# Kernel tuning notes

Measured on AMD Instinct MI355X. Metric: run time of the kernel, lower is better.

The kernel has to match this reference:

```python
import jax, jax.numpy as jnp
import numpy as np

TAU_PLUS = 0.02
TAU_MINUS = 0.02
TAU_X = 0.101
A_TRIPLET = 0.0065
HOMEOSTATIC_RATE = 0.1
DT = 0.001
SPIKE_P = 0.05  # spike probability used to binarize inputs


def setup_inputs() -> dict:
    key = jax.random.key(0)
    k1, k2, k3 = jax.random.split(key, 3)
    B, P, Q, T = 16, 2048, 2048, 256
    pre_spikes = (jax.random.uniform(k1, (B, P, T)) < SPIKE_P).astype(jnp.float32)
    post_spikes = (jax.random.uniform(k2, (B, Q, T)) < SPIKE_P).astype(jnp.float32)
    weights = jax.random.normal(k3, (P, Q), dtype=jnp.float32) * 0.1
    meta_A_plus = jnp.float32(0.01)
    meta_A_minus = jnp.float32(0.012)
    return {"pre_spikes": pre_spikes, "post_spikes": post_spikes,
            "weights": weights, "meta_A_plus": meta_A_plus,
            "meta_A_minus": meta_A_minus}


def _traces(spikes_tbn, decay):
    """Trace value used at step t: x_t = decay * (x_{t-1} + s_{t-1}), x_0 = 0."""
    def step(carry, s):
        x = decay * carry          # decayed trace, used for this step's update
        return x + s, x            # spike added AFTER the update, per original
    init = jnp.zeros(spikes_tbn.shape[1:], spikes_tbn.dtype)
    _, xs = jax.lax.scan(step, init, spikes_tbn)
    return xs  # [T, B, N]


def reference(pre_spikes, post_spikes, weights, meta_A_plus, meta_A_minus):
    B, P, T = pre_spikes.shape
    exp_plus = jnp.exp(jnp.float32(-DT / TAU_PLUS))
    exp_minus = jnp.exp(jnp.float32(-DT / TAU_MINUS))
    exp_x = jnp.exp(jnp.float32(-DT / TAU_X))

    pre_t = jnp.transpose(pre_spikes, (2, 0, 1))    # [T, B, P]
    post_t = jnp.transpose(post_spikes, (2, 0, 1))  # [T, B, Q]

    x_pre = _traces(pre_t, exp_plus)     # [T, B, P]
    x_post = _traces(post_t, exp_minus)  # [T, B, Q]
    x_trip = _traces(post_t, exp_x)      # [T, B, Q]

    # Per-step outer products summed over time == one big contraction over (t, b).
    ltp = jnp.einsum('tbp,tbq->pq', x_pre, post_t) * meta_A_plus
    triplet = jnp.einsum('tbp,tbq->pq', x_pre, post_t * x_trip) * A_TRIPLET
    ltd = jnp.einsum('tbp,tbq->pq', pre_t, x_post) * meta_A_minus
    weight_updates = ltp + triplet - ltd

    # Homeostatic scaling (fresh module: activity history holds only this sample)
    current_activity = (pre_spikes.sum() + post_spikes.sum()) / (B * T)
    scaling_factor = jnp.sqrt(HOMEOSTATIC_RATE / (current_activity + 1e-6))

    updated_weights = weights + weight_updates * scaling_factor
    return jnp.clip(updated_weights, -2.0, 2.0)
```

## Files before the change

### kernel.cpp

```cpp
#include <hip/hip_runtime.h>


constexpr int TB = 16;
constexpr int NP = 2048;
constexpr int NQ = 2048;
constexpr int TT = 256;
constexpr int KH = TB * TT;
constexpr int KT = 2 * KH;

typedef unsigned short ushort_t;
typedef __attribute__((ext_vector_type(8))) __bf16 bf16x8;
typedef __attribute__((ext_vector_type(4))) float f32x4;

__device__ __forceinline__ unsigned bf1(float f) {
    unsigned u = __builtin_bit_cast(unsigned, f);
    return (u + 0x7FFFu + ((u >> 16) & 1u)) >> 16;
}
__device__ __forceinline__ unsigned pack2(float lo, float hi) {
    return bf1(lo) | (bf1(hi) << 16);
}
__device__ __forceinline__ unsigned spk2(float a, float b) {
    return ((a != 0.f) ? 0x3F80u : 0u) | ((b != 0.f) ? 0x3F800000u : 0u);
}

constexpr float DF1 = 0.95122942450071400910f;
constexpr float DF2 = DF1 * DF1;
constexpr float DF4 = DF2 * DF2;
constexpr float DF8 = DF4 * DF4;
constexpr float DF16 = DF8 * DF8;
constexpr float DF32 = DF16 * DF16;
constexpr float DF64 = DF32 * DF32;

constexpr float DX1 = 0.99014786386058731819f;
constexpr float DX2 = DX1 * DX1;
constexpr float DX4 = DX2 * DX2;
constexpr float DX8 = DX4 * DX4;
constexpr float DX16 = DX8 * DX8;
constexpr float DX32 = DX16 * DX16;
constexpr float DX64 = DX32 * DX32;

template <int K>
__device__ __forceinline__ float seg_step(float b, float pw, int sl) {
    float t = __shfl_up(b, K, 64);
    return (sl >= K) ? fmaf(pw, t, b) : b;
}
__device__ __forceinline__ float scan16(float c, float p1, float p2, float p4,
                                        float p8, int sl) {
    c = seg_step<1>(c, p1, sl);
    c = seg_step<2>(c, p2, sl);
    c = seg_step<4>(c, p4, sl);
    c = seg_step<8>(c, p8, sl);
    return c;
}
__device__ __forceinline__ float fold4(float4 u, float d) {
    float C = d * u.x;
    C = d * (C + u.y); C = d * (C + u.z); C = d * (C + u.w);
    return C;
}
__device__ __forceinline__ float4 expand4(float x, float4 u, float d) {
    float4 t;
    t.x = x; x = d * (x + u.x);
    t.y = x; x = d * (x + u.y);
    t.z = x; x = d * (x + u.z);
    t.w = x;
    return t;
}

__global__ __launch_bounds__(256) void stage_traces(
    const float* __restrict__ pre, const float* __restrict__ post,
    const float* __restrict__ mApP, const float* __restrict__ mAmP,
    ushort_t* __restrict__ Ab, ushort_t* __restrict__ Bb,
    float* __restrict__ partials)
{
    const int tid  = threadIdx.x;
    const int lane = tid & 63;
    const int wv   = tid >> 6;
    const int sl   = lane & 15;
    const int rowg = blockIdx.x * 16 + wv * 4 + (lane >> 4);
    const bool isPre = rowg < TB * NP;
    const int m = isPre ? rowg : rowg - TB * NP;
    const int b = m >> 11;
    const int r = m & 2047;

    const float4* srcRow = (const float4*)((isPre ? pre : post) + (size_t)m * TT);
    const float4 u0 = srcRow[sl];
    const float4 u1 = srcRow[16 + sl];
    const float4 u2 = srcRow[32 + sl];
    const float4 u3 = srcRow[48 + sl];

    float cnt = ((u0.x + u0.y) + (u0.z + u0.w)) + ((u1.x + u1.y) + (u1.z + u1.w))
              + ((u2.x + u2.y) + (u2.z + u2.w)) + ((u3.x + u3.y) + (u3.z + u3.w));

    const int hi = lane | 15;

    float bf0 = scan16(fold4(u0, DF1), DF4, DF8, DF16, DF32, sl);
    float bf1_ = scan16(fold4(u1, DF1), DF4, DF8, DF16, DF32, sl);
    float bf2 = scan16(fold4(u2, DF1), DF4, DF8, DF16, DF32, sl);
    float bf3 = scan16(fold4(u3, DF1), DF4, DF8, DF16, DF32, sl);
    const float Tf0 = __shfl(bf0, hi, 64);
    const float Tf1 = __shfl(bf1_, hi, 64);
    const float Tf2 = __shfl(bf2, hi, 64);
    const float Xf1 = Tf0;
    const float Xf2 = fmaf(DF64, Xf1, Tf1);
    const float Xf3 = fmaf(DF64, Xf2, Tf2);
    float ef0 = __shfl_up(bf0, 1, 64);
    float ef1 = __shfl_up(bf1_, 1, 64);
    float ef2 = __shfl_up(bf2, 1, 64);
    float ef3 = __shfl_up(bf3, 1, 64);
    if (sl == 0) { ef0 = 0.f; ef1 = 0.f; ef2 = 0.f; ef3 = 0.f; }
    float pf = 1.f;
    if (sl & 1) pf *= DF4;
    if (sl & 2) pf *= DF8;
    if (sl & 4) pf *= DF16;
    if (sl & 8) pf *= DF32;
    const float4 t0 = expand4(ef0,                 u0, DF1);
    const float4 t1 = expand4(fmaf(pf, Xf1, ef1),  u1, DF1);
    const float4 t2 = expand4(fmaf(pf, Xf2, ef2),  u2, DF1);
    const float4 t3 = expand4(fmaf(pf, Xf3, ef3),  u3, DF1);

    ushort_t* oA = (isPre ? Ab : Bb) + (size_t)r * KT + b * TT + 4 * sl;

    if (isPre) {
        *(uint2*)(oA)            = uint2{pack2(t0.x, t0.y), pack2(t0.z, t0.w)};
        *(uint2*)(oA + 64)       = uint2{pack2(t1.x, t1.y), pack2(t1.z, t1.w)};
        *(uint2*)(oA + 128)      = uint2{pack2(t2.x, t2.y), pack2(t2.z, t2.w)};
        *(uint2*)(oA + 192)      = uint2{pack2(t3.x, t3.y), pack2(t3.z, t3.w)};
        *(uint2*)(oA + KH)       = uint2{spk2(u0.x, u0.y), spk2(u0.z, u0.w)};
        *(uint2*)(oA + KH + 64)  = uint2{spk2(u1.x, u1.y), spk2(u1.z, u1.w)};
        *(uint2*)(oA + KH + 128) = uint2{spk2(u2.x, u2.y), spk2(u2.z, u2.w)};
        *(uint2*)(oA + KH + 192) = uint2{spk2(u3.x, u3.y), spk2(u3.z, u3.w)};
    } else {
        float bx0 = scan16(fold4(u0, DX1), DX4, DX8, DX16, DX32, sl);
        float bx1 = scan16(fold4(u1, DX1), DX4, DX8, DX16, DX32, sl);
        float bx2 = scan16(fold4(u2, DX1), DX4, DX8, DX16, DX32, sl);
        float bx3 = scan16(fold4(u3, DX1), DX4, DX8, DX16, DX32, sl);
        const float Tx0 = __shfl(bx0, hi, 64);
        const float Tx1 = __shfl(bx1, hi, 64);
        const float Tx2 = __shfl(bx2, hi, 64);
        const float Xx1 = Tx0;
        const float Xx2 = fmaf(DX64, Xx1, Tx1);
        const float Xx3 = fmaf(DX64, Xx2, Tx2);
        float ex0 = __shfl_up(bx0, 1, 64);
        float ex1 = __shfl_up(bx1, 1, 64);
        float ex2 = __shfl_up(bx2, 1, 64);
        float ex3 = __shfl_up(bx3, 1, 64);
        if (sl == 0) { ex0 = 0.f; ex1 = 0.f; ex2 = 0.f; ex3 = 0.f; }
        float px = 1.f;
        if (sl & 1) px *= DX4;
        if (sl & 2) px *= DX8;
        if (sl & 4) px *= DX16;
        if (sl & 8) px *= DX32;
        const float4 w0 = expand4(ex0,                u0, DX1);
        const float4 w1 = expand4(fmaf(px, Xx1, ex1), u1, DX1);
        const float4 w2 = expand4(fmaf(px, Xx2, ex2), u2, DX1);
        const float4 w3 = expand4(fmaf(px, Xx3, ex3), u3, DX1);

        const float Ap = *mApP;
        const float Am = *mAmP;
        auto av2 = [&](float sa, float ta, float sb, float tb) -> unsigned {
            unsigned lo = (sa != 0.f) ? bf1(fmaf(0.0065f, ta, Ap)) : 0u;
            unsigned hi2 = (sb != 0.f) ? bf1(fmaf(0.0065f, tb, Ap)) : 0u;
            return lo | (hi2 << 16);
        };
        *(uint2*)(oA)       = uint2{av2(u0.x, w0.x, u0.y, w0.y), av2(u0.z, w0.z, u0.w, w0.w)};
        *(uint2*)(oA + 64)  = uint2{av2(u1.x, w1.x, u1.y, w1.y), av2(u1.z, w1.z, u1.w, w1.w)};
        *(uint2*)(oA + 128) = uint2{av2(u2.x, w2.x, u2.y, w2.y), av2(u2.z, w2.z, u2.w, w2.w)};
        *(uint2*)(oA + 192) = uint2{av2(u3.x, w3.x, u3.y, w3.y), av2(u3.z, w3.z, u3.w, w3.w)};
        *(uint2*)(oA + KH)       = uint2{pack2(-Am * t0.x, -Am * t0.y), pack2(-Am * t0.z, -Am * t0.w)};
        *(uint2*)(oA + KH + 64)  = uint2{pack2(-Am * t1.x, -Am * t1.y), pack2(-Am * t1.z, -Am * t1.w)};
        *(uint2*)(oA + KH + 128) = uint2{pack2(-Am * t2.x, -Am * t2.y), pack2(-Am * t2.z, -Am * t2.w)};
        *(uint2*)(oA + KH + 192) = uint2{pack2(-Am * t3.x, -Am * t3.y), pack2(-Am * t3.z, -Am * t3.w)};
    }

    #pragma unroll
    for (int off = 32; off > 0; off >>= 1)
        cnt += __shfl_down(cnt, off, 64);
    __shared__ float wsum[4];
    if (lane == 0) wsum[wv] = cnt;
    __syncthreads();
    if (tid == 0)
        partials[blockIdx.x] = (wsum[0] + wsum[1]) + (wsum[2] + wsum[3]);
}

__device__ __forceinline__ void async16(const ushort_t* g, ushort_t* l) {
    __builtin_amdgcn_global_load_lds(
        (const __attribute__((address_space(1))) unsigned int*)g,
        (__attribute__((address_space(3))) unsigned int*)l,
        16, 0, 0);
}

#define FENCE() asm volatile("" ::: "memory")
#define BAR()   do { FENCE(); __builtin_amdgcn_s_barrier(); FENCE(); } while (0)
#define LGKM0() asm volatile("s_waitcnt lgkmcnt(0)" ::: "memory")
#define VMC2()  asm volatile("s_waitcnt vmcnt(2)" ::: "memory")
#define VMC0()  asm volatile("s_waitcnt vmcnt(0)" ::: "memory")

#define STAGE(GP, LP, KI, H) do {                                           \
    const ushort_t* _g = (GP) + (size_t)(H) * 128 * KT + (size_t)(KI) * 64; \
    ushort_t* _l = (LP) + (H) * 8192;                                       \
    async16(_g + ofG,  _l + ld0);                                           \
    async16(_g + ofG2, _l + ld1);                                           \
} while (0)

#define RD_A(BUF, QM) do {                                                  \
    _Pragma("unroll")                                                       \
    for (int mi = 0; mi < 4; ++mi) {                                        \
        const ushort_t* _r = &As[BUF][aBase + (QM) * 4096 + mi * 1024];     \
        af[mi][0] = *(const bf16x8*)(_r + sK0);                             \
        af[mi][1] = *(const bf16x8*)(_r + sK1);                             \
    }                                                                       \
} while (0)

#define RD_B(BUF, QN, BV) do {                                              \
    _Pragma("unroll")                                                       \
    for (int ni = 0; ni < 2; ++ni) {                                        \
        const ushort_t* _r = &Bs[BUF][bBase + (QN) * 2048 + ni * 1024];     \
        BV[ni][0] = *(const bf16x8*)(_r + sK0);                             \
        BV[ni][1] = *(const bf16x8*)(_r + sK1);                             \
    }                                                                       \
} while (0)

#define MFMAQ(QM, QN, BV) do {                                              \
    __builtin_amdgcn_s_setprio(1);                                          \
    _Pragma("unroll")                                                       \
    for (int ks = 0; ks < 2; ++ks)                                          \
        _Pragma("unroll")                                                   \
        for (int mi = 0; mi < 4; ++mi)                                      \
            _Pragma("unroll")                                               \
            for (int ni = 0; ni < 2; ++ni)                                  \
                acc[(QM)*4+mi][(QN)*2+ni] =                                 \
                    __builtin_amdgcn_mfma_f32_16x16x32_bf16(                \
                        af[mi][ks], BV[ni][ks],                             \
                        acc[(QM)*4+mi][(QN)*2+ni], 0, 0, 0);                \
    __builtin_amdgcn_s_setprio(0);                                          \
} while (0)

__global__ __launch_bounds__(512) void gemm8(
    const ushort_t* __restrict__ Ab, const ushort_t* __restrict__ Bb,
    const float* __restrict__ sp, float* __restrict__ scaleBuf,
    float* __restrict__ P0, float* __restrict__ P1,
    float* __restrict__ P2, float* __restrict__ P3)
{
    __shared__ ushort_t As[2][256 * 64];
    __shared__ ushort_t Bs[2][256 * 64];
    __shared__ float red[8];

    const int tid  = threadIdx.x;
    const int lane = tid & 63;
    const int wv   = tid >> 6;
    const int wr   = wv >> 2;
    const int wc   = wv & 3;
    const int quad = lane >> 4;
    const int m16  = lane & 15;

    if (blockIdx.x == 0) {
        float v = 0.f;
        #pragma unroll
        for (int i = 0; i < 8; ++i) v += sp[tid + i * 512];
        #pragma unroll
        for (int off = 32; off > 0; off >>= 1)
            v += __shfl_down(v, off, 64);
        if (lane == 0) red[wv] = v;
        __syncthreads();
        if (tid == 0) {
            float s = ((red[0] + red[1]) + (red[2] + red[3]))
                    + ((red[4] + red[5]) + (red[6] + red[7]));
            scaleBuf[0] = sqrtf(0.1f / (s * (1.0f / 4096.0f) + 1e-6f));
        }
    }

    const int id  = blockIdx.x;
    const int xcd = id & 7;
    const int j   = id >> 3;
    const int z   = j & 3;
    const int t   = j >> 2;
    const int pt  = ((xcd >> 1) << 1) | (t >> 2);
    const int qt  = ((xcd & 1) << 2) | (t & 3);
    const int p0  = pt * 256;
    const int q0  = qt * 256;
    const int kbase = z * (KT / 4);

    const ushort_t* Agp = Ab + (size_t)p0 * KT + kbase;
    const ushort_t* Bgp = Bb + (size_t)q0 * KT + kbase;
    const int rIn  = tid >> 3;
    const int rIn2 = rIn + 64;
    const size_t ofG  = (size_t)rIn  * KT + (size_t)((((tid & 7) ^ (rIn  & 7))) * 8);
    const size_t ofG2 = (size_t)rIn2 * KT + (size_t)((((tid & 7) ^ (rIn2 & 7))) * 8);
    const int ld0 = tid * 8;
    const int ld1 = 4096 + tid * 8;

    const int x8  = (m16 & 7) * 8;
    const int sK0 = (quad * 8) ^ x8;
    const int sK1 = ((quad + 4) * 8) ^ x8;
    const int aBase = (wr * 128 + m16) * 64;
    const int bBase = (wc * 64 + m16) * 64;

    f32x4 acc[8][4] = {};
    bf16x8 af[4][2], bv0[2][2], bv1[2][2];

    STAGE(Agp, As[0], 0, 0);
    STAGE(Agp, As[0], 0, 1);
    STAGE(Bgp, Bs[0], 0, 0);
    STAGE(Bgp, Bs[0], 0, 1);
    STAGE(Agp, As[1], 1, 0);
    VMC2();
    BAR();

    #pragma unroll 1
    for (int it = 0; it < 16; ++it) {
        const int k2 = 2 * it;
        RD_A(0, 0);
        RD_B(0, 0, bv0);
        STAGE(Agp, As[1], k2 + 1, 1);
        STAGE(Bgp, Bs[1], k2 + 1, 0);
        BAR(); LGKM0();
        MFMAQ(0, 0, bv0);
        BAR();
        RD_B(0, 1, bv1);
        STAGE(Bgp, Bs[1], k2 + 1, 1);
        BAR(); LGKM0();
        MFMAQ(0, 1, bv1);
        BAR();
        RD_A(0, 1);
        BAR(); LGKM0();
        MFMAQ(1, 1, bv1);
        BAR();
        RD_B(0, 0, bv0);
        if (it < 15) STAGE(Agp, As[0], k2 + 2, 0);
        BAR(); LGKM0();
        MFMAQ(1, 0, bv0);
        if (it < 15) { VMC2(); } else { VMC0(); }
        BAR();
        RD_A(1, 0);
        RD_B(1, 0, bv0);
        if (it < 15) { STAGE(Agp, As[0], k2 + 2, 1); STAGE(Bgp, Bs[0], k2 + 2, 0); }
        BAR(); LGKM0();
        MFMAQ(0, 0, bv0);
        BAR();
        RD_B(1, 1, bv1);
        if (it < 15) STAGE(Bgp, Bs[0], k2 + 2, 1);
        BAR(); LGKM0();
        MFMAQ(0, 1, bv1);
        BAR();
        RD_A(1, 1);
        BAR(); LGKM0();
        MFMAQ(1, 1, bv1);
        BAR();
        RD_B(1, 0, bv0);
        if (it < 15) STAGE(Agp, As[1], k2 + 3, 0);
        BAR(); LGKM0();
        MFMAQ(1, 0, bv0);
        if (it < 15) { VMC2(); }
        BAR();
    }

    float* P = (z == 0) ? P0 : ((z == 1) ? P1 : ((z == 2) ? P2 : P3));
    #pragma unroll
    for (int m = 0; m < 8; ++m) {
        const int prow = p0 + wr * 128 + m * 16 + quad * 4;
        #pragma unroll
        for (int n = 0; n < 4; ++n) {
            const int qcol = q0 + wc * 64 + n * 16 + m16;
            #pragma unroll
            for (int r = 0; r < 4; ++r)
                P[(size_t)(prow + r) * NQ + qcol] = acc[m][n][r];
        }
    }
}

__global__ __launch_bounds__(256, 2) void gemm_split(
    const ushort_t* __restrict__ Ab, const ushort_t* __restrict__ Bb,
    const float* __restrict__ sp, float* __restrict__ scaleBuf,
    float* __restrict__ P0, float* __restrict__ P1)
{
    __shared__ ushort_t Ls[2][128 * 64];
    __shared__ ushort_t Rs[2][128 * 64];
    __shared__ float red[4];

    const int tid  = threadIdx.x;
    const int lane = tid & 63;
    const int wv   = tid >> 6;
    const int wr   = wv >> 1;
    const int wc   = wv & 1;
    const int quad = lane >> 4;
    const int m16  = lane & 15;

    if (blockIdx.x == 0) {
        float v = 0.f;
        #pragma unroll
        for (int i = 0; i < 16; ++i) v += sp[tid + i * 256];
        #pragma unroll
        for (int off = 32; off > 0; off >>= 1)
            v += __shfl_down(v, off, 64);
        if (lane == 0) red[wv] = v;
        __syncthreads();
        if (tid == 0) {
            float s = (red[0] + red[1]) + (red[2] + red[3]);
            scaleBuf[0] = sqrtf(0.1f / (s * (1.0f / 4096.0f) + 1e-6f));
        }
    }

    const int id  = blockIdx.x;
    const int xcd = id & 7;
    const int j5  = id >> 3;
    const int z   = j5 & 1;
    const int t   = j5 >> 1;
    const int pt  = ((xcd >> 1) << 2) + (t >> 3);
    const int qt  = ((xcd & 1) << 3) + (t & 7);

    const int p0 = pt * 128;
    const int q0 = qt * 128;
    const int kbase = z * (KT / 2);
    const int ldsbase = wv * 512;

    const ushort_t* gaP[4];
    const ushort_t* gbP[4];
    #pragma unroll
    for (int rr = 0; rr < 4; ++rr) {
        const int c   = rr * 256 + tid;
        const int row = c >> 3;
        const int kk8 = (c & 7) ^ (row & 7);
        gaP[rr] = Ab + (size_t)(p0 + row) * KT + kbase + kk8 * 8;
        gbP[rr] = Bb + (size_t)(q0 + row) * KT + kbase + kk8 * 8;
    }

    f32x4 acc[4][4] = {};

    auto stageF = [&](int buf) {
        #pragma unroll
        for (int rr = 0; rr < 4; ++rr) {
            async16(gaP[rr], &Ls[buf][rr * 2048 + ldsbase]);
            async16(gbP[rr], &Rs[buf][rr * 2048 + ldsbase]);
            gaP[rr] += 64;
            gbP[rr] += 64;
        }
    };
    auto computeF = [&](int buf) {
        #pragma unroll
        for (int ks = 0; ks < 2; ++ks) {
            bf16x8 afl[4], bfr[4];
            #pragma unroll
            for (int i = 0; i < 4; ++i) {
                const int row  = wr * 64 + i * 16 + m16;
                const int slot = (ks * 4 + quad) ^ (row & 7);
                afl[i] = *(const bf16x8*)&Ls[buf][row * 64 + slot * 8];
            }
            #pragma unroll
            for (int jj = 0; jj < 4; ++jj) {
                const int row  = wc * 64 + jj * 16 + m16;
                const int slot = (ks * 4 + quad) ^ (row & 7);
                bfr[jj] = *(const bf16x8*)&Rs[buf][row * 64 + slot * 8];
            }
            #pragma unroll
            for (int i = 0; i < 4; ++i)
                #pragma unroll
                for (int jj = 0; jj < 4; ++jj)
                    acc[i][jj] = __builtin_amdgcn_mfma_f32_16x16x32_bf16(
                        afl[i], bfr[jj], acc[i][jj], 0, 0, 0);
        }
    };

    constexpr int NIT = (KT / 2) / 64;
    stageF(0);
    for (int kt2 = 0; kt2 < NIT / 2; ++kt2) {
        __syncthreads();
        stageF(1);
        computeF(0);
        __syncthreads();
        if (kt2 + 1 < NIT / 2)
            stageF(0);
        computeF(1);
    }

    float* P = z ? P1 : P0;
    #pragma unroll
    for (int i = 0; i < 4; ++i) {
        const int prow = p0 + wr * 64 + i * 16 + quad * 4;
        #pragma unroll
        for (int jj = 0; jj < 4; ++jj) {
            const int qcol = q0 + wc * 64 + jj * 16 + m16;
            #pragma unroll
            for (int r2 = 0; r2 < 4; ++r2)
                P[(size_t)(prow + r2) * NQ + qcol] = acc[i][jj][r2];
        }
    }
}

__global__ __launch_bounds__(256) void merge_out4(
    const float* __restrict__ W, const float* __restrict__ P1,
    const float* __restrict__ P2, const float* __restrict__ P3,
    const float* __restrict__ scaleBuf, float* __restrict__ Out)
{
    const float scale = scaleBuf[0];
    const size_t i4 = (size_t)blockIdx.x * 256 + threadIdx.x;
    float4 w = ((const float4*)W)[i4];
    float4 a = ((const float4*)Out)[i4];
    float4 b = ((const float4*)P1)[i4];
    float4 c = ((const float4*)P2)[i4];
    float4 d = ((const float4*)P3)[i4];
    float4 o;
    o.x = fminf(fmaxf(fmaf(scale, (a.x + b.x) + (c.x + d.x), w.x), -2.f), 2.f);
    o.y = fminf(fmaxf(fmaf(scale, (a.y + b.y) + (c.y + d.y), w.y), -2.f), 2.f);
    o.z = fminf(fmaxf(fmaf(scale, (a.z + b.z) + (c.z + d.z), w.z), -2.f), 2.f);
    o.w = fminf(fmaxf(fmaf(scale, (a.w + b.w) + (c.w + d.w), w.w), -2.f), 2.f);
    ((float4*)Out)[i4] = o;
}

__global__ __launch_bounds__(256) void merge_out2(
    const float* __restrict__ W, const float* __restrict__ P1,
    const float* __restrict__ scaleBuf, float* __restrict__ Out)
{
    const float scale = scaleBuf[0];
    const size_t i4 = (size_t)blockIdx.x * 256 + threadIdx.x;
    float4 w = ((const float4*)W)[i4];
    float4 a = ((const float4*)Out)[i4];
    float4 c = ((const float4*)P1)[i4];
    float4 o;
    o.x = fminf(fmaxf(fmaf(scale, a.x + c.x, w.x), -2.f), 2.f);
    o.y = fminf(fmaxf(fmaf(scale, a.y + c.y, w.y), -2.f), 2.f);
    o.z = fminf(fmaxf(fmaf(scale, a.z + c.z, w.z), -2.f), 2.f);
    o.w = fminf(fmaxf(fmaf(scale, a.w + c.w, w.w), -2.f), 2.f);
    ((float4*)Out)[i4] = o;
}

extern "C" void kernel_launch(void* const* d_in, const int* in_sizes, int n_in,
                              void* d_out, int out_size, void* d_ws, size_t ws_size,
                              hipStream_t stream) {
    const float* pre  = (const float*)d_in[0];
    const float* post = (const float*)d_in[1];
    const float* W    = (const float*)d_in[2];
    const float* mAp  = (const float*)d_in[3];
    const float* mAm  = (const float*)d_in[4];
    float* out = (float*)d_out;

    const size_t AB = (size_t)NP * KT * 2;
    const size_t PB = (size_t)NP * NQ * 4;

    char* ws = (char*)d_ws;
    float* partials = (float*)ws;
    float* scaleBuf = (float*)(ws + 16384);
    ushort_t* Ab = (ushort_t*)(ws + 32768);
    ushort_t* Bb = (ushort_t*)(ws + 32768 + AB);
    float* P1 = (float*)(ws + 32768 + 2 * AB);
    float* P2 = (float*)(ws + 32768 + 2 * AB + PB);
    float* P3 = (float*)(ws + 32768 + 2 * AB + 2 * PB);

    stage_traces<<<dim3((TB * NP + TB * NQ) / 16), dim3(256), 0, stream>>>(
        pre, post, mAp, mAm, Ab, Bb, partials);

    if (ws_size >= 32768 + 2 * AB + 3 * PB) {
        gemm8<<<dim3(256), dim3(512), 0, stream>>>(
            Ab, Bb, partials, scaleBuf, out, P1, P2, P3);
        merge_out4<<<dim3(NP * NQ / 1024), dim3(256), 0, stream>>>(
            W, P1, P2, P3, scaleBuf, out);
    } else {
        gemm_split<<<dim3(512), dim3(256), 0, stream>>>(
            Ab, Bb, partials, scaleBuf, out, P1);
        merge_out2<<<dim3(NP * NQ / 1024), dim3(256), 0, stream>>>(
            W, P1, scaleBuf, out);
    }
}
```

Baseline: 209.7 us.

## Remap warp tiles across LDS halves and deepen async prefetch schedule

Each warp's sub-tile is remapped so its quadrant reads land in the staged 128-row halves, letting a half-tile be refilled as soon as its last reader is done. The whole next k-slice is now prefetched in the prologue and the wait threshold is raised so more global-to-LDS loads are in flight. One redundant B fragment reload per half-iteration is dropped by reusing bv0. This deepens memory/compute overlap, in exchange for more outstanding loads and a changed output index mapping that must match the new layout.

```diff
diff --git a/kernel.cpp b/kernel.cpp
--- a/kernel.cpp
+++ b/kernel.cpp
@@ -192,7 +192,7 @@
 #define FENCE() asm volatile("" ::: "memory")
 #define BAR()   do { FENCE(); __builtin_amdgcn_s_barrier(); FENCE(); } while (0)
 #define LGKM0() asm volatile("s_waitcnt lgkmcnt(0)" ::: "memory")
-#define VMC2()  asm volatile("s_waitcnt vmcnt(2)" ::: "memory")
+#define VMC8()  asm volatile("s_waitcnt vmcnt(8)" ::: "memory")
 #define VMC0()  asm volatile("s_waitcnt vmcnt(0)" ::: "memory")
 
 #define STAGE(GP, LP, KI, H) do {                                           \
@@ -205,7 +205,7 @@
 #define RD_A(BUF, QM) do {                                                  \
     _Pragma("unroll")                                                       \
     for (int mi = 0; mi < 4; ++mi) {                                        \
-        const ushort_t* _r = &As[BUF][aBase + (QM) * 4096 + mi * 1024];     \
+        const ushort_t* _r = &As[BUF][(QM) * 8192 + aBase + mi * 1024];     \
         af[mi][0] = *(const bf16x8*)(_r + sK0);                             \
         af[mi][1] = *(const bf16x8*)(_r + sK1);                             \
     }                                                                       \
@@ -214,7 +214,7 @@
 #define RD_B(BUF, QN, BV) do {                                              \
     _Pragma("unroll")                                                       \
     for (int ni = 0; ni < 2; ++ni) {                                        \
-        const ushort_t* _r = &Bs[BUF][bBase + (QN) * 2048 + ni * 1024];     \
+        const ushort_t* _r = &Bs[BUF][(QN) * 8192 + bBase + ni * 1024];     \
         BV[ni][0] = *(const bf16x8*)(_r + sK0);                             \
         BV[ni][1] = *(const bf16x8*)(_r + sK1);                             \
     }                                                                       \
@@ -292,8 +292,8 @@
     const int x8  = (m16 & 7) * 8;
     const int sK0 = (quad * 8) ^ x8;
     const int sK1 = ((quad + 4) * 8) ^ x8;
-    const int aBase = (wr * 128 + m16) * 64;
-    const int bBase = (wc * 64 + m16) * 64;
+    const int aBase = (wr * 64 + m16) * 64;
+    const int bBase = (wc * 32 + m16) * 64;
 
     f32x4 acc[8][4] = {};
     bf16x8 af[4][2], bv0[2][2], bv1[2][2];
@@ -303,64 +303,65 @@
     STAGE(Bgp, Bs[0], 0, 0);
     STAGE(Bgp, Bs[0], 0, 1);
     STAGE(Agp, As[1], 1, 0);
-    VMC2();
+    STAGE(Agp, As[1], 1, 1);
+    STAGE(Bgp, Bs[1], 1, 0);
+    STAGE(Bgp, Bs[1], 1, 1);
+    VMC8();
     BAR();
 
     #pragma unroll 1
     for (int it = 0; it < 16; ++it) {
         const int k2 = 2 * it;
+        const bool pf = (it < 15);
         RD_A(0, 0);
         RD_B(0, 0, bv0);
-        STAGE(Agp, As[1], k2 + 1, 1);
-        STAGE(Bgp, Bs[1], k2 + 1, 0);
         BAR(); LGKM0();
         MFMAQ(0, 0, bv0);
         BAR();
         RD_B(0, 1, bv1);
-        STAGE(Bgp, Bs[1], k2 + 1, 1);
+        if (pf) { STAGE(Agp, As[0], k2 + 2, 0); STAGE(Bgp, Bs[0], k2 + 2, 0); }
         BAR(); LGKM0();
         MFMAQ(0, 1, bv1);
         BAR();
         RD_A(0, 1);
+        if (pf) STAGE(Bgp, Bs[0], k2 + 2, 1);
         BAR(); LGKM0();
         MFMAQ(1, 1, bv1);
         BAR();
-        RD_B(0, 0, bv0);
-        if (it < 15) STAGE(Agp, As[0], k2 + 2, 0);
-        BAR(); LGKM0();
+        if (pf) STAGE(Agp, As[0], k2 + 2, 1);
+        BAR();
         MFMAQ(1, 0, bv0);
-        if (it < 15) { VMC2(); } else { VMC0(); }
+        if (pf) { VMC8(); } else { VMC0(); }
         BAR();
         RD_A(1, 0);
         RD_B(1, 0, bv0);
-        if (it < 15) { STAGE(Agp, As[0], k2 + 2, 1); STAGE(Bgp, Bs[0], k2 + 2, 0); }
         BAR(); LGKM0();
         MFMAQ(0, 0, bv0);
         BAR();
         RD_B(1, 1, bv1);
-        if (it < 15) STAGE(Bgp, Bs[0], k2 + 2, 1);
+        if (pf) { STAGE(Agp, As[1], k2 + 3, 0); STAGE(Bgp, Bs[1], k2 + 3, 0); }
         BAR(); LGKM0();
         MFMAQ(0, 1, bv1);
         BAR();
         RD_A(1, 1);
+        if (pf) STAGE(Bgp, Bs[1], k2 + 3, 1);
         BAR(); LGKM0();
         MFMAQ(1, 1, bv1);
         BAR();
-        RD_B(1, 0, bv0);
-        if (it < 15) STAGE(Agp, As[1], k2 + 3, 0);
-        BAR(); LGKM0();
+        if (pf) STAGE(Agp, As[1], k2 + 3, 1);
+        BAR();
         MFMAQ(1, 0, bv0);
-        if (it < 15) { VMC2(); }
+        if (pf) { VMC8(); }
         BAR();
     }
 
     float* P = (z == 0) ? P0 : ((z == 1) ? P1 : ((z == 2) ? P2 : P3));
     #pragma unroll
     for (int m = 0; m < 8; ++m) {
-        const int prow = p0 + wr * 128 + m * 16 + quad * 4;
+        const int prow = p0 + ((m >> 2) << 7) + wr * 64 + (m & 3) * 16 + quad * 4;
         #pragma unroll
         for (int n = 0; n < 4; ++n) {
-            const int qcol = q0 + wc * 64 + n * 16 + m16;
+            const int qcol = q0 + ((n >> 1) << 7) + wc * 32 + (n & 1) * 16 + m16;
             #pragma unroll
             for (int r = 0; r < 4; ++r)
                 P[(size_t)(prow + r) * NQ + qcol] = acc[m][n][r];
```

Result: faster. 200.1 us (-4.6%).
